# Performance work log

Measured on AMD Instinct MI355X. Metric: run time of the kernel, lower is better.

Reference implementation:

```python
import jax, jax.numpy as jnp
import numpy as np

B, T, D_LAT = 128, 256, 256
N_HIDDEN = 1024
H_SMALL = N_HIDDEN // 2  # 512: lstm1/lstm2 hidden size
H_BIG = N_HIDDEN         # 1024: lstm3 hidden size


def _p(key, shape, scale=0.05):
    return (jax.random.normal(key, shape, dtype=jnp.float32) * scale)


def setup_inputs() -> dict:
    key = jax.random.key(0)
    ks = jax.random.split(key, 16)
    return {
        "X": jax.random.normal(ks[0], (B, T, D_LAT), dtype=jnp.float32),
        # LSTMCell 1: input D_LAT -> hidden H_SMALL (torch layout: [4H, in])
        "W_ih1": _p(ks[1], (4 * H_SMALL, D_LAT)),
        "W_hh1": _p(ks[2], (4 * H_SMALL, H_SMALL)),
        "b_ih1": _p(ks[3], (4 * H_SMALL,)),
        "b_hh1": _p(ks[4], (4 * H_SMALL,)),
        # LSTMCell 2: H_SMALL -> H_SMALL
        "W_ih2": _p(ks[5], (4 * H_SMALL, H_SMALL)),
        "W_hh2": _p(ks[6], (4 * H_SMALL, H_SMALL)),
        "b_ih2": _p(ks[7], (4 * H_SMALL,)),
        "b_hh2": _p(ks[8], (4 * H_SMALL,)),
        # LSTMCell 3: H_SMALL -> H_BIG
        "W_ih3": _p(ks[9], (4 * H_BIG, H_SMALL)),
        "W_hh3": _p(ks[10], (4 * H_BIG, H_BIG)),
        "b_ih3": _p(ks[11], (4 * H_BIG,)),
        "b_hh3": _p(ks[12], (4 * H_BIG,)),
        # Linear: H_BIG -> D_LAT (torch layout: [out, in])
        "W_lin": _p(ks[13], (D_LAT, H_BIG)),
        "b_lin": _p(ks[14], (D_LAT,)),
    }


def _lstm_cell(x, h, c, W_ih, W_hh, b_ih, b_hh):
    # torch.nn.LSTMCell gate order: i, f, g, o
    gates = x @ W_ih.T + b_ih + h @ W_hh.T + b_hh  # [B, 4H]
    i, f, g, o = jnp.split(gates, 4, axis=-1)
    c_new = jax.nn.sigmoid(f) * c + jax.nn.sigmoid(i) * jnp.tanh(g)
    h_new = jax.nn.sigmoid(o) * jnp.tanh(c_new)
    return h_new, c_new


def reference(X, W_ih1, W_hh1, b_ih1, b_hh1,
              W_ih2, W_hh2, b_ih2, b_hh2,
              W_ih3, W_hh3, b_ih3, b_hh3,
              W_lin, b_lin):
    n = X.shape[0]
    z_s = jnp.zeros((n, H_SMALL), dtype=X.dtype)
    z_b = jnp.zeros((n, H_BIG), dtype=X.dtype)
    init = (z_s, z_s, z_s, z_s, z_b, z_b)

    def step(carry, x_t):
        h1, c1, h2, c2, h3, c3 = carry
        h1, c1 = _lstm_cell(x_t, h1, c1, W_ih1, W_hh1, b_ih1, b_hh1)
        h2, c2 = _lstm_cell(h1, h2, c2, W_ih2, W_hh2, b_ih2, b_hh2)
        h3, c3 = _lstm_cell(h2, h3, c3, W_ih3, W_hh3, b_ih3, b_hh3)
        out = h3 @ W_lin.T + b_lin  # [B, D_LAT]
        return (h1, c1, h2, c2, h3, c3), out

    xs = jnp.swapaxes(X, 0, 1)  # [T, B, D_LAT]
    _, outputs = jax.lax.scan(step, init, xs)
    return outputs  # [T, B, D_LAT] == torch.stack(outputs) with future=0
```

## Files before the change

kernel.cpp:

```cpp
#include <hip/hip_runtime.h>
#include <stdint.h>

#define NWG 208
#define NPHASE 259

typedef __attribute__((ext_vector_type(8))) short short8;
typedef __attribute__((ext_vector_type(4))) float floatx4;
typedef __attribute__((ext_vector_type(4))) unsigned int uintx4;

static constexpr int Bb = 128, Tt = 256, Dl = 256, Hs = 512, Hb = 1024;

static constexpr size_t OFF_FLAGS = 0;
static constexpr size_t OFF_B1  = 1024;
static constexpr size_t OFF_B2  = OFF_B1 + 2048*4;
static constexpr size_t OFF_B3  = OFF_B2 + 2048*4;
static constexpr size_t OFF_BL  = OFF_B3 + 4096*4;
static constexpr size_t OFF_W1  = OFF_BL + 1024;
static constexpr size_t OFF_W2  = OFF_W1 + (size_t)2048*768*2;
static constexpr size_t OFF_W3  = OFF_W2 + (size_t)2048*1024*2;
static constexpr size_t OFF_WL  = OFF_W3 + (size_t)4096*1536*2;
static constexpr size_t FIXED_END = OFF_WL + (size_t)256*1024*2;

template<int D> struct Lay {
  static constexpr size_t H1  = FIXED_END;
  static constexpr size_t H2  = H1 + (size_t)D*Bb*Hs*2;
  static constexpr size_t H3  = H2 + (size_t)D*Bb*Hs*2;
  static constexpr size_t XB  = H3 + (size_t)D*Bb*Hb*2;
  static constexpr size_t END = XB + (size_t)D*Bb*Dl*2;
};

static constexpr int SMEM_BYTES = 135168;
static constexpr int STG_OFF    = 131072;

__device__ __forceinline__ unsigned short f2bf(float f) {
  unsigned int u = __float_as_uint(f);
  unsigned int r = (u + 0x7fffu + ((u >> 16) & 1u)) >> 16;
  return (unsigned short)r;
}
__device__ __forceinline__ float sigm(float x) { return 1.f/(1.f + __expf(-x)); }
__device__ __forceinline__ float tanh_f(float x) {
  x = fminf(fmaxf(x, -15.f), 15.f);
  float e = __expf(-2.f*x);
  return (1.f - e)/(1.f + e);
}
__device__ __forceinline__ size_t blk_off(int row, int u) {
  return ((size_t)(u >> 5)*8 + (row >> 4))*512 + (size_t)((u & 31) >> 3)*128
       + (size_t)(row & 15)*8 + (u & 7);
}
__device__ __forceinline__ void st_dword_cg(void* p, unsigned int v) {
  asm volatile("global_store_dword %0, %1, off sc0 sc1" :: "v"(p), "v"(v) : "memory");
}
__device__ __forceinline__ void st_b128_cg(void* p, uintx4 v) {
  asm volatile("global_store_dwordx4 %0, %1, off sc0 sc1" :: "v"(p), "v"(v) : "memory");
}
__device__ __forceinline__ void waitcnt_vm0() {
  asm volatile("s_waitcnt vmcnt(0)" ::: "memory");
}

template<int D>
__global__ void lstm_init(
    const float* __restrict__ X,
    const float* __restrict__ Wih1, const float* __restrict__ Whh1,
    const float* __restrict__ bih1, const float* __restrict__ bhh1,
    const float* __restrict__ Wih2, const float* __restrict__ Whh2,
    const float* __restrict__ bih2, const float* __restrict__ bhh2,
    const float* __restrict__ Wih3, const float* __restrict__ Whh3,
    const float* __restrict__ bih3, const float* __restrict__ bhh3,
    const float* __restrict__ Wlin, const float* __restrict__ blin,
    unsigned char* __restrict__ ws)
{
  size_t i0 = (size_t)blockIdx.x*blockDim.x + threadIdx.x;
  size_t np = (size_t)gridDim.x*blockDim.x;

  unsigned int* fl = (unsigned int*)(ws + OFF_FLAGS);
  for (size_t i = i0; i < 256; i += np) fl[i] = (i < NWG) ? 0u : 0xFFFFFFFFu;

  float* b1 = (float*)(ws + OFF_B1);
  float* b2 = (float*)(ws + OFF_B2);
  float* b3 = (float*)(ws + OFF_B3);
  float* bl = (float*)(ws + OFF_BL);
  for (size_t i = i0; i < 2048; i += np) b1[i] = bih1[i] + bhh1[i];
  for (size_t i = i0; i < 2048; i += np) b2[i] = bih2[i] + bhh2[i];
  for (size_t i = i0; i < 4096; i += np) b3[i] = bih3[i] + bhh3[i];
  for (size_t i = i0; i < 256;  i += np) bl[i] = blin[i];

  unsigned short* w1 = (unsigned short*)(ws + OFF_W1);
  unsigned short* w2 = (unsigned short*)(ws + OFF_W2);
  unsigned short* w3 = (unsigned short*)(ws + OFF_W3);
  unsigned short* wl = (unsigned short*)(ws + OFF_WL);
  for (size_t i = i0; i < (size_t)2048*768; i += np) {
    size_t r = i/768, k = i - r*768;
    float v = (k < 256) ? Wih1[r*256 + k] : Whh1[r*512 + (k - 256)];
    w1[i] = f2bf(v);
  }
  for (size_t i = i0; i < (size_t)2048*1024; i += np) {
    size_t r = i >> 10, k = i & 1023;
    float v = (k < 512) ? Wih2[r*512 + k] : Whh2[r*512 + (k - 512)];
    w2[i] = f2bf(v);
  }
  for (size_t i = i0; i < (size_t)4096*1536; i += np) {
    size_t r = i/1536, k = i - r*1536;
    float v = (k < 512) ? Wih3[r*512 + k] : Whh3[r*1024 + (k - 512)];
    w3[i] = f2bf(v);
  }
  for (size_t i = i0; i < (size_t)256*1024; i += np) wl[i] = f2bf(Wlin[i]);

  unsigned short* rings = (unsigned short*)(ws + Lay<D>::H1);
  const size_t nring = (size_t)D*Bb*Hs + (size_t)D*Bb*Hs + (size_t)D*Bb*Hb;
  for (size_t i = i0; i < nring; i += np) rings[i] = 0;

  unsigned short* xb0 = (unsigned short*)(ws + Lay<D>::XB);
  for (size_t i = i0; i < (size_t)Bb*Dl; i += np) {
    size_t b = i >> 8, d = i & 255;
    xb0[blk_off((int)b, (int)d)] = f2bf(X[(b*(size_t)Tt + 0)*Dl + d]);
  }
}

template<int TYPE>
__device__ __forceinline__ void layer_phase(
    const unsigned short* __restrict__ segA,
    const unsigned short* __restrict__ segB,
    unsigned short* __restrict__ hout,
    unsigned char* __restrict__ smem,
    const float* __restrict__ bias_r,
    float (&creg)[4][2][4],
    int U0, int wv, int lane, int tid)
{
  constexpr int K    = (TYPE==0 ? 768 : TYPE==1 ? 1024 : 1536);
  constexpr int KB1  = (TYPE==0 ? 256 : 512);
  constexpr int MF   = (TYPE==2 ? 2 : 4);
  constexpr int NCH  = K/128;
  const int l15 = lane & 15;
  const int klo = (lane >> 4) << 3;
  const int g   = l15 >> 2;
  const int mbase = (TYPE==2 ? wv*32 : (wv&1)*64);
  const int nfb   = (TYPE==2 ? 0 : (wv>>1)*2);

  const size_t lof = (size_t)(lane >> 4)*128 + (size_t)l15*8;
  const unsigned short* pa[MF];
  const unsigned short* pb[MF];
  #pragma unroll
  for (int mf = 0; mf < MF; ++mf) {
    const size_t rb = (size_t)((mbase >> 4) + mf)*512;
    pa[mf] = segA + rb + lof;
    pb[mf] = segB + rb + lof;
  }
  int rowbyte[2], xr[2];
  #pragma unroll
  for (int nf = 0; nf < 2; ++nf) {
    const int rp = (nfb + nf)*16 + l15;
    rowbyte[nf] = rp*(K*2);
    xr[nf] = (rp & 7) << 4;
  }
  const int klobyte = klo*2;

  floatx4 acc[MF][2];
  #pragma unroll
  for (int mf = 0; mf < MF; ++mf)
    #pragma unroll
    for (int nf = 0; nf < 2; ++nf) {
      float bv = bias_r[nf];
      floatx4 b4 = {bv, bv, bv, bv};
      acc[mf][nf] = b4;
    }

  short8 A0[4][MF], A1[4][MF];
  auto LOADC = [&](int c, short8 (&A)[4][MF]) {
    #pragma unroll
    for (int ks = 0; ks < 4; ++ks) {
      const int kb = c*128 + ks*32;
      #pragma unroll
      for (int mf = 0; mf < MF; ++mf) {
        const unsigned short* p = (kb < KB1)
            ? pa[mf] + (size_t)(kb >> 5)*4096
            : pb[mf] + (size_t)((kb - KB1) >> 5)*4096;
        A[ks][mf] = *(const short8*)p;
      }
    }
  };
  auto MM = [&](int c, short8 (&A)[4][MF]) {
    #pragma unroll
    for (int ks = 0; ks < 4; ++ks) {
      const int kb = c*128 + ks*32;
      short8 bf[2];
      #pragma unroll
      for (int nf = 0; nf < 2; ++nf)
        bf[nf] = *(const short8*)(smem + rowbyte[nf] + ((kb*2 + klobyte) ^ xr[nf]));
      #pragma unroll
      for (int mf = 0; mf < MF; ++mf)
        #pragma unroll
        for (int nf = 0; nf < 2; ++nf)
          acc[mf][nf] = __builtin_amdgcn_mfma_f32_16x16x32_bf16(A[ks][mf], bf[nf], acc[mf][nf], 0, 0, 0);
    }
  };

  LOADC(0, A0);
  #pragma unroll 1
  for (int ch = 0; ch < NCH; ch += 2) {
    LOADC(ch + 1, A1);
    MM(ch, A0);
    if (ch + 2 < NCH) LOADC(ch + 2, A0);
    MM(ch + 1, A1);
  }

  unsigned short* stg = (unsigned short*)(smem + STG_OFF);
  const int a = (U0 & 31) >> 3;
  #pragma unroll
  for (int nf = 0; nf < 2; ++nf) {
    const int u = U0 + (nfb + nf)*4 + (l15 & 3);
    #pragma unroll
    for (int mf = 0; mf < MF; ++mf) {
      float h4[4];
      #pragma unroll
      for (int j = 0; j < 4; ++j) {
        float s0  = acc[mf][nf][j];
        float s4  = __shfl_xor(s0, 4);
        float s8  = __shfl_xor(s0, 8);
        float s12 = __shfl_xor(s0, 12);
        float iv = (g==0)?s0 :(g==1)?s4 :(g==2)?s8 :s12;
        float fv = (g==0)?s4 :(g==1)?s0 :(g==2)?s12:s8;
        float gv = (g==0)?s8 :(g==1)?s12:(g==2)?s0 :s4;
        float ov = (g==0)?s12:(g==1)?s8 :(g==2)?s4 :s0;
        float c  = sigm(fv)*creg[mf][nf][j] + sigm(iv)*tanh_f(gv);
        creg[mf][nf][j] = c;
        h4[j] = sigm(ov)*tanh_f(c);
      }
      float hs = (g==0)?h4[0]:(g==1)?h4[1]:(g==2)?h4[2]:h4[3];
      const int row = mbase + mf*16 + ((lane >> 4) << 2) + g;
      const int c2  = (TYPE==2) ? (row >> 4)
                                : ((row >> 4)*2 + (((u & 31) >> 3) - a));
      stg[c2*128 + (row & 15)*8 + (u & 7)] = f2bf(hs);
    }
  }
  __syncthreads();

  const size_t gbase = (size_t)(U0 >> 5)*4096;
  if (TYPE == 2) {
    if (tid < 128) {
      const int c2 = tid >> 4, w = tid & 15;
      short8 v = *(const short8*)(stg + c2*128 + w*8);
      st_b128_cg(hout + gbase + (size_t)c2*512 + (size_t)a*128 + w*8, *(uintx4*)&v);
    }
  } else {
    const int c2 = tid >> 4, w = tid & 15;
    short8 v = *(const short8*)(stg + c2*128 + w*8);
    st_b128_cg(hout + gbase + (size_t)(c2 >> 1)*512 + (size_t)(a + (c2 & 1))*128 + w*8, *(uintx4*)&v);
  }
}

template<int D>
__global__ void __launch_bounds__(256, 1)
lstm_persist(const float* __restrict__ X, float* __restrict__ out,
             unsigned char* __restrict__ ws)
{
  extern __shared__ unsigned char smem[];

  __builtin_amdgcn_fence(__ATOMIC_ACQUIRE, "agent");

  const int tid  = threadIdx.x;
  const int lane = tid & 63;
  const int wv   = tid >> 6;
  const int wg   = blockIdx.x;
  const int l15  = lane & 15;

  unsigned int* flags = (unsigned int*)(ws + OFF_FLAGS);
  const float* bias1 = (const float*)(ws + OFF_B1);
  const float* bias2 = (const float*)(ws + OFF_B2);
  const float* bias3 = (const float*)(ws + OFF_B3);
  const float* biasl = (const float*)(ws + OFF_BL);
  const unsigned short* W1 = (const unsigned short*)(ws + OFF_W1);
  const unsigned short* W2 = (const unsigned short*)(ws + OFF_W2);
  const unsigned short* W3 = (const unsigned short*)(ws + OFF_W3);
  const unsigned short* WL = (const unsigned short*)(ws + OFF_WL);
  unsigned short* h1r = (unsigned short*)(ws + Lay<D>::H1);
  unsigned short* h2r = (unsigned short*)(ws + Lay<D>::H2);
  unsigned short* h3r = (unsigned short*)(ws + Lay<D>::H3);
  unsigned short* Xb  = (unsigned short*)(ws + Lay<D>::XB);

  auto slot = [](int t) -> size_t { return (size_t)(t & (D - 1)); };
  const size_t HSs = (size_t)Bb*Hs, HBs = (size_t)Bb*Hb, XBs = (size_t)Bb*Dl;

  int type, U0 = 0, osec = 0, K = 0, WROWS = 0, HGATE = 0;
  const unsigned short* Wg = nullptr; const float* biasp = nullptr;
  if (wg < 32)        { type = 0; U0 = wg*16;        Wg = W1; biasp = bias1; K = 768;  WROWS = 64; HGATE = 512; }
  else if (wg < 64)   { type = 1; U0 = (wg-32)*16;   Wg = W2; biasp = bias2; K = 1024; WROWS = 64; HGATE = 512; }
  else if (wg < 192)  { type = 2; U0 = (wg-64)*8;    Wg = W3; biasp = bias3; K = 1536; WROWS = 32; HGATE = 1024; }
  else                { type = 3; osec = (wg-192)*16; Wg = WL; K = 1024; WROWS = 16; }

  {
    const int rowchunks = K >> 3;
    for (int idx = tid; idx < WROWS*rowchunks; idx += 256) {
      const int rp = idx / rowchunks, kc = idx - rp*rowchunks;
      int R;
      if (type == 3) R = osec + rp;
      else {
        const int c = rp & 15;
        R = (c >> 2)*HGATE + U0 + (rp >> 4)*4 + (c & 3);
      }
      uintx4 v = *(const uintx4*)(Wg + (size_t)R*K + kc*8);
      const int db = rp*(K*2) + ((kc*16) ^ ((rp & 7) << 4));
      *(uintx4*)(smem + db) = v;
    }
  }

  float bias_r[2] = {0.f, 0.f};
  if (type < 3) {
    const int g   = l15 >> 2;
    const int nfb = (type == 2 ? 0 : (wv >> 1)*2);
    #pragma unroll
    for (int nf = 0; nf < 2; ++nf) {
      const int u = U0 + (nfb + nf)*4 + (l15 & 3);
      bias_r[nf] = biasp[g*HGATE + u];
    }
  } else {
    bias_r[0] = biasl[osec + l15];
  }

  float creg[4][2][4];
  #pragma unroll
  for (int a = 0; a < 4; ++a)
    #pragma unroll
    for (int b = 0; b < 2; ++b)
      #pragma unroll
      for (int c = 0; c < 4; ++c) creg[a][b][c] = 0.f;

  __syncthreads();

  for (int p = 0; p < NPHASE; ++p) {
    if (type == 0) {
      const int t = p;
      if (t < Tt)
        layer_phase<0>(Xb + slot(t)*XBs,
                       h1r + slot(t-1)*HSs,
                       h1r + slot(t)*HSs,
                       smem, bias_r, creg, U0, wv, lane, tid);
    } else if (type == 1) {
      const int t = p - 1;
      if (t >= 0 && t < Tt)
        layer_phase<1>(h1r + slot(t)*HSs,
                       h2r + slot(t-1)*HSs,
                       h2r + slot(t)*HSs,
                       smem, bias_r, creg, U0, wv, lane, tid);
    } else if (type == 2) {
      const int t = p - 2;
      if (t >= 0 && t < Tt)
        layer_phase<2>(h2r + slot(t)*HSs,
                       h3r + slot(t-1)*HBs,
                       h3r + slot(t)*HBs,
                       smem, bias_r, creg, U0, wv, lane, tid);
    } else {
      if (p + 1 < Tt) {
        const int tx = p + 1;
        const int j = wg - 192;
        const int i = tid*8;
        const int row = j*8 + (i >> 8);
        const int d = i & 255;
        const float* xp = X + ((size_t)row*Tt + tx)*Dl + d;
        float4 f0 = *(const float4*)xp;
        float4 f1 = *(const float4*)(xp + 4);
        uintx4 pk;
        pk[0] = (unsigned int)f2bf(f0.x) | ((unsigned int)f2bf(f0.y) << 16);
        pk[1] = (unsigned int)f2bf(f0.z) | ((unsigned int)f2bf(f0.w) << 16);
        pk[2] = (unsigned int)f2bf(f1.x) | ((unsigned int)f2bf(f1.y) << 16);
        pk[3] = (unsigned int)f2bf(f1.z) | ((unsigned int)f2bf(f1.w) << 16);
        st_b128_cg(Xb + slot(tx)*XBs + blk_off(row, d), pk);
      }
      const int to = p - 3;
      if (to >= 0 && to < Tt) {
        const unsigned short* hA = h3r + slot(to)*HBs;
        const size_t lof = (size_t)(lane >> 4)*128 + (size_t)l15*8;
        const unsigned short* pa[2];
        #pragma unroll
        for (int mf = 0; mf < 2; ++mf)
          pa[mf] = hA + (size_t)((wv*32 + mf*16) >> 4)*512 + lof;
        const int rowbyte = l15*2048;
        const int xr = (l15 & 7) << 4;
        const int klobyte = ((lane >> 4) << 3)*2;
        floatx4 oacc[2];
        {
          floatx4 b4 = {bias_r[0], bias_r[0], bias_r[0], bias_r[0]};
          oacc[0] = b4; oacc[1] = b4;
        }
        short8 A0[4][2], A1[4][2];
        auto HLOAD = [&](int c, short8 (&A)[4][2]) {
          #pragma unroll
          for (int ks = 0; ks < 4; ++ks)
            #pragma unroll
            for (int mf = 0; mf < 2; ++mf)
              A[ks][mf] = *(const short8*)(pa[mf] + (size_t)(c*4 + ks)*4096);
        };
        auto HMM = [&](int c, short8 (&A)[4][2]) {
          #pragma unroll
          for (int ks = 0; ks < 4; ++ks) {
            const int kb = c*128 + ks*32;
            short8 bw = *(const short8*)(smem + rowbyte + ((kb*2 + klobyte) ^ xr));
            #pragma unroll
            for (int mf = 0; mf < 2; ++mf)
              oacc[mf] = __builtin_amdgcn_mfma_f32_16x16x32_bf16(A[ks][mf], bw, oacc[mf], 0, 0, 0);
          }
        };
        HLOAD(0, A0);
        #pragma unroll 1
        for (int ch = 0; ch < 8; ch += 2) {
          HLOAD(ch + 1, A1);
          HMM(ch, A0);
          if (ch + 2 < 8) HLOAD(ch + 2, A0);
          HMM(ch + 1, A1);
        }
        const int col = osec + l15;
        #pragma unroll
        for (int mf = 0; mf < 2; ++mf) {
          const int b0 = wv*32 + mf*16 + ((lane >> 4) << 2);
          #pragma unroll
          for (int j = 0; j < 4; ++j)
            st_dword_cg(out + ((size_t)to*Bb + b0 + j)*Dl + col,
                        __float_as_uint(oacc[mf][j]));
        }
      }
    }

    if (p < NPHASE - 1) {
      waitcnt_vm0();
      __syncthreads();
      const unsigned int tgt = (unsigned int)(p + 1);
      if (tid == 0) st_dword_cg(flags + wg, tgt);
      if (tid < 64) {
        uintx4 f;
        for (;;) {
          asm volatile("global_load_dwordx4 %0, %1, off sc0 sc1\n\t"
                       "s_waitcnt vmcnt(0)"
                       : "=v"(f) : "v"(flags + lane*4) : "memory");
          if (f[0] >= tgt && f[1] >= tgt && f[2] >= tgt && f[3] >= tgt) break;
          __builtin_amdgcn_s_sleep(4);
        }
      }
      __syncthreads();
      if (D == 2 || (p & 7) == 7)
        __builtin_amdgcn_fence(__ATOMIC_ACQUIRE, "agent");
    }
  }
}

extern "C" void kernel_launch(void* const* d_in, const int* in_sizes, int n_in,
                              void* d_out, int out_size, void* d_ws, size_t ws_size,
                              hipStream_t stream)
{
  const float* X    = (const float*)d_in[0];
  const float* Wih1 = (const float*)d_in[1];
  const float* Whh1 = (const float*)d_in[2];
  const float* bih1 = (const float*)d_in[3];
  const float* bhh1 = (const float*)d_in[4];
  const float* Wih2 = (const float*)d_in[5];
  const float* Whh2 = (const float*)d_in[6];
  const float* bih2 = (const float*)d_in[7];
  const float* bhh2 = (const float*)d_in[8];
  const float* Wih3 = (const float*)d_in[9];
  const float* Whh3 = (const float*)d_in[10];
  const float* bih3 = (const float*)d_in[11];
  const float* bhh3 = (const float*)d_in[12];
  const float* Wlin = (const float*)d_in[13];
  const float* blin = (const float*)d_in[14];
  unsigned char* ws = (unsigned char*)d_ws;

  if (ws_size >= Lay<8>::END) {
    lstm_init<8><<<2048, 256, 0, stream>>>(X, Wih1, Whh1, bih1, bhh1,
                                           Wih2, Whh2, bih2, bhh2,
                                           Wih3, Whh3, bih3, bhh3,
                                           Wlin, blin, ws);
    lstm_persist<8><<<NWG, 256, SMEM_BYTES, stream>>>(X, (float*)d_out, ws);
  } else if (ws_size >= Lay<2>::END) {
    lstm_init<2><<<2048, 256, 0, stream>>>(X, Wih1, Whh1, bih1, bhh1,
                                           Wih2, Whh2, bih2, bhh2,
                                           Wih3, Whh3, bih3, bhh3,
                                           Wlin, blin, ws);
    lstm_persist<2><<<NWG, 256, SMEM_BYTES, stream>>>(X, (float*)d_out, ws);
  }
}
```

Measured before the change: 4.014 ms.

## Double workgroup size to 512 threads and split per-wave GEMM tiles in half

The persistent LSTM kernel now launches 512 threads per workgroup instead of 256, so each wave covers half as many batch rows (MF halved) and the gate, weight-load and output-projection loops are remapped to the eight waves. TYPE 2 layers use longer K chunks so each wave does more MFMAs per load batch. The aim is more latency hiding and more MFMA issue parallelism per CU within each serialized timestep. The cost is higher register pressure under the new launch bounds and a larger __syncthreads group in every phase, which could slow the per-step barrier.

```diff
diff --git a/kernel.cpp b/kernel.cpp
--- a/kernel.cpp
+++ b/kernel.cpp
@@ -123,18 +123,18 @@
     unsigned short* __restrict__ hout,
     unsigned char* __restrict__ smem,
     const float* __restrict__ bias_r,
-    float (&creg)[4][2][4],
+    float (&creg)[2][2][4],
     int U0, int wv, int lane, int tid)
 {
   constexpr int K    = (TYPE==0 ? 768 : TYPE==1 ? 1024 : 1536);
   constexpr int KB1  = (TYPE==0 ? 256 : 512);
-  constexpr int MF   = (TYPE==2 ? 2 : 4);
-  constexpr int NCH  = K/128;
+  constexpr int MF   = (TYPE==2 ? 1 : 2);
+  constexpr int CKS  = (TYPE==2 ? 8 : 4);
+  constexpr int NCH  = K/(32*CKS);
   const int l15 = lane & 15;
-  const int klo = (lane >> 4) << 3;
   const int g   = l15 >> 2;
-  const int mbase = (TYPE==2 ? wv*32 : (wv&1)*64);
-  const int nfb   = (TYPE==2 ? 0 : (wv>>1)*2);
+  const int mbase = (TYPE==2 ? wv*16 : (wv&3)*32);
+  const int nfb   = (TYPE==2 ? 0 : (wv>>2)*2);
 
   const size_t lof = (size_t)(lane >> 4)*128 + (size_t)l15*8;
   const unsigned short* pa[MF];
@@ -152,7 +152,7 @@
     rowbyte[nf] = rp*(K*2);
     xr[nf] = (rp & 7) << 4;
   }
-  const int klobyte = klo*2;
+  const int klobyte = ((lane >> 4) << 3)*2;
 
   floatx4 acc[MF][2];
   #pragma unroll
@@ -164,11 +164,11 @@
       acc[mf][nf] = b4;
     }
 
-  short8 A0[4][MF], A1[4][MF];
-  auto LOADC = [&](int c, short8 (&A)[4][MF]) {
-    #pragma unroll
-    for (int ks = 0; ks < 4; ++ks) {
-      const int kb = c*128 + ks*32;
+  short8 A0[CKS][MF], A1[CKS][MF];
+  auto LOADC = [&](int c, short8 (&A)[CKS][MF]) {
+    #pragma unroll
+    for (int ks = 0; ks < CKS; ++ks) {
+      const int kb = (c*CKS + ks)*32;
       #pragma unroll
       for (int mf = 0; mf < MF; ++mf) {
         const unsigned short* p = (kb < KB1)
@@ -178,10 +178,10 @@
       }
     }
   };
-  auto MM = [&](int c, short8 (&A)[4][MF]) {
-    #pragma unroll
-    for (int ks = 0; ks < 4; ++ks) {
-      const int kb = c*128 + ks*32;
+  auto MM = [&](int c, short8 (&A)[CKS][MF]) {
+    #pragma unroll
+    for (int ks = 0; ks < CKS; ++ks) {
+      const int kb = (c*CKS + ks)*32;
       short8 bf[2];
       #pragma unroll
       for (int nf = 0; nf < 2; ++nf)
@@ -242,14 +242,16 @@
       st_b128_cg(hout + gbase + (size_t)c2*512 + (size_t)a*128 + w*8, *(uintx4*)&v);
     }
   } else {
-    const int c2 = tid >> 4, w = tid & 15;
-    short8 v = *(const short8*)(stg + c2*128 + w*8);
-    st_b128_cg(hout + gbase + (size_t)(c2 >> 1)*512 + (size_t)(a + (c2 & 1))*128 + w*8, *(uintx4*)&v);
+    if (tid < 256) {
+      const int c2 = tid >> 4, w = tid & 15;
+      short8 v = *(const short8*)(stg + c2*128 + w*8);
+      st_b128_cg(hout + gbase + (size_t)(c2 >> 1)*512 + (size_t)(a + (c2 & 1))*128 + w*8, *(uintx4*)&v);
+    }
   }
 }
 
 template<int D>
-__global__ void __launch_bounds__(256, 1)
+__global__ void __launch_bounds__(512, 2)
 lstm_persist(const float* __restrict__ X, float* __restrict__ out,
              unsigned char* __restrict__ ws)
 {
@@ -289,7 +291,7 @@
 
   {
     const int rowchunks = K >> 3;
-    for (int idx = tid; idx < WROWS*rowchunks; idx += 256) {
+    for (int idx = tid; idx < WROWS*rowchunks; idx += 512) {
       const int rp = idx / rowchunks, kc = idx - rp*rowchunks;
       int R;
       if (type == 3) R = osec + rp;
@@ -306,7 +308,7 @@
   float bias_r[2] = {0.f, 0.f};
   if (type < 3) {
     const int g   = l15 >> 2;
-    const int nfb = (type == 2 ? 0 : (wv >> 1)*2);
+    const int nfb = (type == 2 ? 0 : (wv >> 2)*2);
     #pragma unroll
     for (int nf = 0; nf < 2; ++nf) {
       const int u = U0 + (nfb + nf)*4 + (l15 & 3);
@@ -316,9 +318,9 @@
     bias_r[0] = biasl[osec + l15];
   }
 
-  float creg[4][2][4];
+  float creg[2][2][4];
   #pragma unroll
-  for (int a = 0; a < 4; ++a)
+  for (int a = 0; a < 2; ++a)
     #pragma unroll
     for (int b = 0; b < 2; ++b)
       #pragma unroll
@@ -349,7 +351,7 @@
                        h3r + slot(t)*HBs,
                        smem, bias_r, creg, U0, wv, lane, tid);
     } else {
-      if (p + 1 < Tt) {
+      if (p + 1 < Tt && tid < 256) {
         const int tx = p + 1;
         const int j = wg - 192;
         const int i = tid*8;
@@ -369,34 +371,24 @@
       if (to >= 0 && to < Tt) {
         const unsigned short* hA = h3r + slot(to)*HBs;
         const size_t lof = (size_t)(lane >> 4)*128 + (size_t)l15*8;
-        const unsigned short* pa[2];
-        #pragma unroll
-        for (int mf = 0; mf < 2; ++mf)
-          pa[mf] = hA + (size_t)((wv*32 + mf*16) >> 4)*512 + lof;
+        const unsigned short* pa0 = hA + (size_t)wv*512 + lof;
         const int rowbyte = l15*2048;
         const int xr = (l15 & 7) << 4;
         const int klobyte = ((lane >> 4) << 3)*2;
-        floatx4 oacc[2];
-        {
-          floatx4 b4 = {bias_r[0], bias_r[0], bias_r[0], bias_r[0]};
-          oacc[0] = b4; oacc[1] = b4;
-        }
-        short8 A0[4][2], A1[4][2];
-        auto HLOAD = [&](int c, short8 (&A)[4][2]) {
+        floatx4 oacc;
+        { floatx4 b4 = {bias_r[0], bias_r[0], bias_r[0], bias_r[0]}; oacc = b4; }
+        short8 A0[4], A1[4];
+        auto HLOAD = [&](int c, short8 (&A)[4]) {
           #pragma unroll
           for (int ks = 0; ks < 4; ++ks)
-            #pragma unroll
-            for (int mf = 0; mf < 2; ++mf)
-              A[ks][mf] = *(const short8*)(pa[mf] + (size_t)(c*4 + ks)*4096);
+            A[ks] = *(const short8*)(pa0 + (size_t)(c*4 + ks)*4096);
         };
-        auto HMM = [&](int c, short8 (&A)[4][2]) {
+        auto HMM = [&](int c, short8 (&A)[4]) {
           #pragma unroll
           for (int ks = 0; ks < 4; ++ks) {
             const int kb = c*128 + ks*32;
             short8 bw = *(const short8*)(smem + rowbyte + ((kb*2 + klobyte) ^ xr));
-            #pragma unroll
-            for (int mf = 0; mf < 2; ++mf)
-              oacc[mf] = __builtin_amdgcn_mfma_f32_16x16x32_bf16(A[ks][mf], bw, oacc[mf], 0, 0, 0);
+            oacc = __builtin_amdgcn_mfma_f32_16x16x32_bf16(A[ks], bw, oacc, 0, 0, 0);
           }
         };
         HLOAD(0, A0);
@@ -408,14 +400,11 @@
           HMM(ch + 1, A1);
         }
         const int col = osec + l15;
+        const int b0 = wv*16 + ((lane >> 4) << 2);
         #pragma unroll
-        for (int mf = 0; mf < 2; ++mf) {
-          const int b0 = wv*32 + mf*16 + ((lane >> 4) << 2);
-          #pragma unroll
-          for (int j = 0; j < 4; ++j)
-            st_dword_cg(out + ((size_t)to*Bb + b0 + j)*Dl + col,
-                        __float_as_uint(oacc[mf][j]));
-        }
+        for (int j = 0; j < 4; ++j)
+          st_dword_cg(out + ((size_t)to*Bb + b0 + j)*Dl + col,
+                      __float_as_uint(oacc[j]));
       }
     }
 
@@ -467,12 +456,12 @@
                                            Wih2, Whh2, bih2, bhh2,
                                            Wih3, Whh3, bih3, bhh3,
                                            Wlin, blin, ws);
-    lstm_persist<8><<<NWG, 256, SMEM_BYTES, stream>>>(X, (float*)d_out, ws);
+    lstm_persist<8><<<NWG, 512, SMEM_BYTES, stream>>>(X, (float*)d_out, ws);
   } else if (ws_size >= Lay<2>::END) {
     lstm_init<2><<<2048, 256, 0, stream>>>(X, Wih1, Whh1, bih1, bhh1,
                                            Wih2, Whh2, bih2, bhh2,
                                            Wih3, Whh3, bih3, bhh3,
                                            Wlin, blin, ws);
-    lstm_persist<2><<<NWG, 256, SMEM_BYTES, stream>>>(X, (float*)d_out, ws);
-  }
-}
+    lstm_persist<2><<<NWG, 512, SMEM_BYTES, stream>>>(X, (float*)d_out, ws);
+  }
+}
```

New measurement: 3.812 ms. -5.0%, faster.
